# Kernel optimization log

Measured on AMD Instinct MI355X. Metric: run time of the kernel, lower is better.

## Reference

```python
import jax, jax.numpy as jnp
import numpy as np

B, D, H, NG = 8192, 2048, 2048, 7  # batch, input_size, hidden_size, num gate networks


def setup_inputs() -> dict:
    key = jax.random.key(0)
    ks = jax.random.split(key, 7)
    hx = jax.random.normal(ks[0], (B, D), dtype=jnp.float32)
    cx1 = jax.random.normal(ks[1], (B, H), dtype=jnp.float32)
    cx2 = jax.random.normal(ks[2], (B, H), dtype=jnp.float32)
    tj = jax.random.uniform(ks[3], (B, 1), dtype=jnp.float32)
    dt = jax.random.uniform(ks[4], (B, 1), dtype=jnp.float32)
    # fused weights for the 7 gate/decay networks, order: i1,i2,f1,f2,o,z,d
    W = jax.random.normal(ks[5], (D, NG * H), dtype=jnp.float32) * (1.0 / np.sqrt(D))
    b = jax.random.normal(ks[6], (NG * H,), dtype=jnp.float32) * 0.01
    return {"hx": hx, "cx1": cx1, "cx2": cx2, "tj": tj, "dt": dt, "W": W, "b": b}


def reference(hx, cx1, cx2, tj, dt, W, b):
    # One fused GEMM for all 7 gate networks, then split.
    g = hx @ W + b  # [B, 7H]
    i1, i2, f1, f2, o, z_raw, d_raw = [g[:, k * H:(k + 1) * H] for k in range(NG)]
    sig = jax.nn.sigmoid
    i1, i2, f1, f2, o = sig(i1), sig(i2), sig(f1), sig(f2), sig(o)
    z = jnp.tanh(z_raw)                 # Tanh(LC_z(hx)) as in forward
    decay = jax.nn.softplus(d_raw)      # Decay_network: positive decay coeff
    cy1 = f1 * cx1 + i1 * z             # fast cell state
    cy2 = f2 * cx2 + i2 * z             # asymptotic cell state
    t = tj + dt
    # continuous-time decay: c(t) = cy2 + (cy1 - cy2) * exp(-decay * (t - tj))
    c_t = cy2 + (cy1 - cy2) * jnp.exp(-decay * (t - tj))
    h_t = o * jnp.tanh(c_t)             # get_h(t)
    return jnp.stack([cy1, cy2, h_t])   # [3, B, H]
```

## Files before the change

### kernel.cpp

```cpp
#include <hip/hip_runtime.h>
#include <hip/hip_bf16.h>
#include <stdint.h>


#define B_SZ 8192
#define D_SZ 2048
#define H_SZ 2048
#define NG   7
#define NW   (NG * H_SZ)
#define BM   256
#define BN   32
#define BK   32
#define NKST (D_SZ / BK)
#define NBX  (B_SZ / BM)
#define NBY  (H_SZ / BN)

#define WB_BYTES   ((size_t)NBY * NKST * 14336)
#define HXB_OFF    WB_BYTES
#define HXB_BYTES  ((size_t)NBX * NKST * 16384)
#define WS_NEEDED  (WB_BYTES + HXB_BYTES)

typedef __attribute__((ext_vector_type(8))) short bf16x8;
typedef __attribute__((ext_vector_type(4))) float f32x4;

__device__ __forceinline__ uint32_t cvtpk(float lo, float hi) {
    uint32_t r;
    asm("v_cvt_pk_bf16_f32 %0, %1, %2" : "=v"(r) : "v"(lo), "v"(hi));
    return r;
}
__device__ __forceinline__ void glds16(const void* g, void* l) {
    __builtin_amdgcn_global_load_lds(
        (const __attribute__((address_space(1))) uint32_t*)g,
        (__attribute__((address_space(3))) uint32_t*)l, 16, 0, 0);
}
__device__ __forceinline__ float sigmoidf_(float x) {
    return 1.0f / (1.0f + __expf(-x));
}
__device__ __forceinline__ float tanhf_(float x) {
    float ax = fabsf(x);
    float e = __expf(2.0f * ax);
    float t = 1.0f - 2.0f / (e + 1.0f);
    return copysignf(t, x);
}
__device__ __forceinline__ float softplusf_(float x) {
    return (x > 30.0f) ? x : __logf(1.0f + __expf(x));
}

__global__ __launch_bounds__(896) void conv_w(const float* __restrict__ W,
                                              char* __restrict__ wb)
{
    const int by = blockIdx.x >> 6;
    const int ks = blockIdx.x & 63;
    const int u  = threadIdx.x;
    const int r  = u >> 2;
    const int pc = u & 3;
    const int koct = pc ^ ((r >> 1) & 3);
    const int g  = r >> 5;
    const int n  = r & 31;
    const int col = g * H_SZ + by * BN + n;
    const float* src = W + (size_t)(ks * BK + koct * 8) * NW + col;
    float w0 = src[0];
    float w1 = src[(size_t)NW];
    float w2 = src[(size_t)2 * NW];
    float w3 = src[(size_t)3 * NW];
    float w4 = src[(size_t)4 * NW];
    float w5 = src[(size_t)5 * NW];
    float w6 = src[(size_t)6 * NW];
    float w7 = src[(size_t)7 * NW];
    uint4 o;
    o.x = cvtpk(w0, w1); o.y = cvtpk(w2, w3);
    o.z = cvtpk(w4, w5); o.w = cvtpk(w6, w7);
    *(uint4*)(wb + (size_t)blockIdx.x * 14336 + u * 16) = o;
}

__global__ __launch_bounds__(1024) void conv_hx(const float* __restrict__ hx,
                                                char* __restrict__ hxb)
{
    const int bx = blockIdx.x >> 6;
    const int ks = blockIdx.x & 63;
    const int u  = threadIdx.x;
    const int r  = u >> 2;
    const int pc = u & 3;
    const int koct = pc ^ ((r >> 1) & 3);
    const float* src = hx + (size_t)(bx * BM + r) * D_SZ + ks * BK + koct * 8;
    f32x4 a = *(const f32x4*)(src);
    f32x4 b = *(const f32x4*)(src + 4);
    uint4 o;
    o.x = cvtpk(a[0], a[1]); o.y = cvtpk(a[2], a[3]);
    o.z = cvtpk(b[0], b[1]); o.w = cvtpk(b[2], b[3]);
    *(uint4*)(hxb + (size_t)blockIdx.x * 16384 + u * 16) = o;
}

#define NTH3 512
#define BUFB 30720
#define NBUF 4

#define SB0 __builtin_amdgcn_sched_barrier(0)
#define WAIT_LGKM0 do {                                          \
    asm volatile("s_waitcnt lgkmcnt(0)" ::: "memory");           \
    SB0; } while (0)
#define WAIT_VM(N) do {                                          \
    asm volatile("s_waitcnt vmcnt(" #N ")" ::: "memory");        \
    __builtin_amdgcn_s_barrier();                                \
    SB0; } while (0)

__global__ __launch_bounds__(NTH3, 2) void lstm_bf16(
    const char* __restrict__ wb, const char* __restrict__ hxb,
    const float* __restrict__ cx1, const float* __restrict__ cx2,
    const float* __restrict__ dt, const float* __restrict__ bias,
    float* __restrict__ out)
{
    __shared__ char smem[NBUF * BUFB];

    const int tid  = threadIdx.x;
    const int lane = tid & 63;
    const int wid  = tid >> 6;
    const int wm   = wid >> 1;
    const int wn   = wid & 1;
    const int l15  = lane & 15;
    const int lg   = lane >> 4;

    const int b0  = blockIdx.x;
    const int swz = (b0 & 7) * 256 + (b0 >> 3);
    const int by2 = swz >> 6;
    const int rem = swz & 63;
    const int bx  = rem >> 1;
    const int by  = by2 * 2 + (rem & 1);
    const int gm0 = bx * BM;
    const int n0  = by * BN;

    const size_t hx_tile0 = (size_t)(bx * NKST) << 14;
    const size_t w_tile0  = (size_t)(by * NKST) * 14336;

    const int xch = (lg ^ ((l15 >> 1) & 3)) * 8;
    const uint32_t aAb = (uint32_t)(uintptr_t)(smem) + 2u * ((wm * 64 + l15) * 32 + xch);
    const uint32_t aBb = (uint32_t)(uintptr_t)(smem) + 16384u + 2u * ((wn * 16 + l15) * 32 + xch);
    const uint32_t aA0 = aAb,            aA1 = aAb + BUFB;
    const uint32_t aA2 = aAb + 2 * BUFB, aA3 = aAb + 3 * BUFB;
    const uint32_t aB0 = aBb,            aB1 = aBb + BUFB;
    const uint32_t aB2 = aBb + 2 * BUFB, aB3 = aBb + 3 * BUFB;

    const int lane16 = lane << 4;
    const char* hxp0 = hxb + hx_tile0 + (wid << 11) + lane16;
    const char* wbp0 = wb + w_tile0 + wid * 1792 + lane16;
    char* dA0 = smem + (wid << 11);            char* dB0 = smem + 16384 + wid * 1792;
    char* dA1 = dA0 + BUFB;                    char* dB1 = dB0 + BUFB;
    char* dA2 = dA0 + 2 * BUFB;                char* dB2 = dB0 + 2 * BUFB;
    char* dA3 = dA0 + 3 * BUFB;                char* dB3 = dB0 + 3 * BUFB;

    f32x4 acc[NG][4];
    #pragma unroll
    for (int g = 0; g < NG; ++g)
        #pragma unroll
        for (int mf = 0; mf < 4; ++mf)
            acc[g][mf] = (f32x4){0.f, 0.f, 0.f, 0.f};

    bf16x8 fA[2][4];
    bf16x8 fB[2][7];

    #define ISSUE_FRAGS(S, AA, AB) do {                                           \
        asm volatile("s_mov_b32 m0, -1" ::);                                      \
        asm volatile("ds_read_b128 %0, %1"                : "=v"(fA[S][0]) : "v"(AA)); \
        asm volatile("ds_read_b128 %0, %1 offset:1024"    : "=v"(fA[S][1]) : "v"(AA)); \
        asm volatile("ds_read_b128 %0, %1 offset:2048"    : "=v"(fA[S][2]) : "v"(AA)); \
        asm volatile("ds_read_b128 %0, %1 offset:3072"    : "=v"(fA[S][3]) : "v"(AA)); \
        asm volatile("ds_read_b128 %0, %1"                : "=v"(fB[S][0]) : "v"(AB)); \
        asm volatile("ds_read_b128 %0, %1 offset:2048"    : "=v"(fB[S][1]) : "v"(AB)); \
        asm volatile("ds_read_b128 %0, %1 offset:4096"    : "=v"(fB[S][2]) : "v"(AB)); \
        asm volatile("ds_read_b128 %0, %1 offset:6144"    : "=v"(fB[S][3]) : "v"(AB)); \
        asm volatile("ds_read_b128 %0, %1 offset:8192"    : "=v"(fB[S][4]) : "v"(AB)); \
        asm volatile("ds_read_b128 %0, %1 offset:10240"   : "=v"(fB[S][5]) : "v"(AB)); \
        asm volatile("ds_read_b128 %0, %1 offset:12288"   : "=v"(fB[S][6]) : "v"(AB)); \
        SB0; } while (0)

    #define CLUSTER(S) do {                                                       \
        __builtin_amdgcn_s_setprio(1);                                            \
        _Pragma("unroll")                                                         \
        for (int g_ = 0; g_ < NG; ++g_)                                           \
            _Pragma("unroll")                                                     \
            for (int mf_ = 0; mf_ < 4; ++mf_)                                     \
                acc[g_][mf_] = __builtin_amdgcn_mfma_f32_16x16x32_bf16(           \
                    fA[S][mf_], fB[S][g_], acc[g_][mf_], 0, 0, 0);                \
        __builtin_amdgcn_s_setprio(0);                                            \
        SB0; } while (0)

    #define STAGE_C(c) do {                                                       \
        glds16(hxp, dA##c); glds16(hxp + 1024, dA##c + 1024);                     \
        glds16(wbp, dB##c);                                                       \
        if (lane < 48) glds16(wbp + 1024, dB##c + 1024);                          \
        hxp += 16384; wbp += 14336; } while (0)

    #define STAGE_K(c, k) do {                                                    \
        glds16(hxp0 + (k) * 16384, dA##c);                                        \
        glds16(hxp0 + (k) * 16384 + 1024, dA##c + 1024);                          \
        glds16(wbp0 + (k) * 14336, dB##c);                                        \
        if (lane < 48) glds16(wbp0 + (k) * 14336 + 1024, dB##c + 1024);           \
    } while (0)

    #define K_STEP(CN, SCUR, SNXT, VMN, STG) do {                                 \
        WAIT_LGKM0;                 \
        WAIT_VM(VMN);               \
        ISSUE_FRAGS(SNXT, aA##CN, aB##CN);                                        \
        STG;                                                                      \
        SB0;                                                                      \
        CLUSTER(SCUR); } while (0)

    STAGE_K(0, 0);
    STAGE_K(1, 1);
    STAGE_K(2, 2);
    const char* hxp = hxp0 + 3 * 16384;
    const char* wbp = wbp0 + 3 * 14336;
    asm volatile("s_waitcnt vmcnt(8)" ::: "memory");
    __builtin_amdgcn_s_barrier();
    SB0;
    ISSUE_FRAGS(0, aA0, aB0);

    #pragma unroll 1
    for (int it = 0; it < 15; ++it) {
        K_STEP(1, 0, 1, 4, STAGE_C(3));
        K_STEP(2, 1, 0, 4, STAGE_C(0));
        K_STEP(3, 0, 1, 4, STAGE_C(1));
        K_STEP(0, 1, 0, 4, STAGE_C(2));
    }
    K_STEP(1, 0, 1, 4, STAGE_C(3));
    K_STEP(2, 1, 0, 4, (void)0);
    K_STEP(3, 0, 1, 0, (void)0);
    WAIT_LGKM0;
    CLUSTER(1);

    const size_t BH = (size_t)B_SZ * H_SZ;
    const int j = n0 + wn * 16 + l15;
    float bj[NG];
    #pragma unroll
    for (int g = 0; g < NG; ++g) bj[g] = bias[g * H_SZ + j];

    #pragma unroll
    for (int mf = 0; mf < 4; ++mf) {
        #pragma unroll
        for (int r = 0; r < 4; ++r) {
            int row = gm0 + wm * 64 + mf * 16 + lg * 4 + r;
            float dtv = dt[row];
            float i1 = sigmoidf_(acc[0][mf][r] + bj[0]);
            float i2 = sigmoidf_(acc[1][mf][r] + bj[1]);
            float f1 = sigmoidf_(acc[2][mf][r] + bj[2]);
            float f2 = sigmoidf_(acc[3][mf][r] + bj[3]);
            float o  = sigmoidf_(acc[4][mf][r] + bj[4]);
            float z  = tanhf_(acc[5][mf][r] + bj[5]);
            float dec = softplusf_(acc[6][mf][r] + bj[6]);
            size_t idx = (size_t)row * H_SZ + j;
            float c1 = cx1[idx], c2 = cx2[idx];
            float cy1 = f1 * c1 + i1 * z;
            float cy2 = f2 * c2 + i2 * z;
            float ct  = cy2 + (cy1 - cy2) * __expf(-dec * dtv);
            float ht  = o * tanhf_(ct);
            out[idx]          = cy1;
            out[BH + idx]     = cy2;
            out[2 * BH + idx] = ht;
        }
    }
}

#define NTH  512
#define LDP  40
__global__ __launch_bounds__(NTH, 2) void lstm_f32(
    const float* __restrict__ hx, const float* __restrict__ cx1,
    const float* __restrict__ cx2, const float* __restrict__ dt,
    const float* __restrict__ W, const float* __restrict__ bias,
    float* __restrict__ out)
{
    __shared__ ushort sA[BM * LDP];
    __shared__ ushort sB[NG * BN * LDP];

    const int tid = threadIdx.x;
    const int nwg = gridDim.x;
    const int cpx = nwg >> 3;
    const int b0  = blockIdx.x;
    const int swz = (b0 & 7) * cpx + (b0 >> 3);
    const int bx  = swz & 31;
    const int by  = swz >> 5;
    const int gm0 = bx * BM;
    const int n0  = by * BN;

    const int lane = tid & 63;
    const int wid  = tid >> 6;
    const int wm   = wid >> 1;
    const int wn   = wid & 1;
    const int l15  = lane & 15;
    const int lg   = lane >> 4;

    const int ar0 = tid >> 2,          aq0 = tid & 3;
    const int ar1 = (tid + 512) >> 2,  aq1 = tid & 3;
    const bool hasB = (tid < 448);
    const int bg  = tid >> 6;
    const int bkq = (tid >> 3) & 7;
    const int bnq = tid & 7;

    f32x4 pa[4];
    f32x4 pb[4];

    auto issue_loads = [&](int K0) {
        {
            const float* p = hx + (size_t)(gm0 + ar0) * D_SZ + K0 + aq0 * 8;
            pa[0] = *(const f32x4*)(p);
            pa[1] = *(const f32x4*)(p + 4);
        }
        {
            const float* p = hx + (size_t)(gm0 + ar1) * D_SZ + K0 + aq1 * 8;
            pa[2] = *(const f32x4*)(p);
            pa[3] = *(const f32x4*)(p + 4);
        }
        if (hasB) {
            const float* p = W + (size_t)(K0 + bkq * 4) * NW + bg * H_SZ + n0 + bnq * 4;
            pb[0] = *(const f32x4*)(p);
            pb[1] = *(const f32x4*)(p + NW);
            pb[2] = *(const f32x4*)(p + 2 * NW);
            pb[3] = *(const f32x4*)(p + 3 * NW);
        }
    };

    auto store_lds = [&]() {
        {
            uint4 u;
            u.x = cvtpk(pa[0][0], pa[0][1]); u.y = cvtpk(pa[0][2], pa[0][3]);
            u.z = cvtpk(pa[1][0], pa[1][1]); u.w = cvtpk(pa[1][2], pa[1][3]);
            *(uint4*)(&sA[ar0 * LDP + aq0 * 8]) = u;
        }
        {
            uint4 u;
            u.x = cvtpk(pa[2][0], pa[2][1]); u.y = cvtpk(pa[2][2], pa[2][3]);
            u.z = cvtpk(pa[3][0], pa[3][1]); u.w = cvtpk(pa[3][2], pa[3][3]);
            *(uint4*)(&sA[ar1 * LDP + aq1 * 8]) = u;
        }
        if (hasB) {
            #pragma unroll
            for (int jj = 0; jj < 4; ++jj) {
                uint2 v;
                v.x = cvtpk(pb[0][jj], pb[1][jj]);
                v.y = cvtpk(pb[2][jj], pb[3][jj]);
                *(uint2*)(&sB[(bg * BN + bnq * 4 + jj) * LDP + bkq * 4]) = v;
            }
        }
    };

    f32x4 acc[NG][4];
    #pragma unroll
    for (int g = 0; g < NG; ++g)
        #pragma unroll
        for (int mf = 0; mf < 4; ++mf)
            acc[g][mf] = (f32x4){0.f, 0.f, 0.f, 0.f};

    int aoff[4];
    #pragma unroll
    for (int mf = 0; mf < 4; ++mf)
        aoff[mf] = (wm * 64 + mf * 16 + l15) * LDP + lg * 8;
    int boff[NG];
    #pragma unroll
    for (int g = 0; g < NG; ++g)
        boff[g] = (g * BN + wn * 16 + l15) * LDP + lg * 8;

    issue_loads(0);
    for (int kk = 0; kk < NKST; ++kk) {
        store_lds();
        __syncthreads();
        if (kk + 1 < NKST) issue_loads((kk + 1) * BK);

        bf16x8 af[4];
        #pragma unroll
        for (int mf = 0; mf < 4; ++mf)
            af[mf] = *(const bf16x8*)(&sA[aoff[mf]]);
        #pragma unroll
        for (int g = 0; g < NG; ++g) {
            bf16x8 bfr = *(const bf16x8*)(&sB[boff[g]]);
            #pragma unroll
            for (int mf = 0; mf < 4; ++mf)
                acc[g][mf] = __builtin_amdgcn_mfma_f32_16x16x32_bf16(
                    af[mf], bfr, acc[g][mf], 0, 0, 0);
        }
        __syncthreads();
    }

    const size_t BH = (size_t)B_SZ * H_SZ;
    const int j = n0 + wn * 16 + l15;
    float bj[NG];
    #pragma unroll
    for (int g = 0; g < NG; ++g) bj[g] = bias[g * H_SZ + j];

    #pragma unroll
    for (int mf = 0; mf < 4; ++mf) {
        #pragma unroll
        for (int r = 0; r < 4; ++r) {
            int row = gm0 + wm * 64 + mf * 16 + lg * 4 + r;
            float dtv = dt[row];
            float i1 = sigmoidf_(acc[0][mf][r] + bj[0]);
            float i2 = sigmoidf_(acc[1][mf][r] + bj[1]);
            float f1 = sigmoidf_(acc[2][mf][r] + bj[2]);
            float f2 = sigmoidf_(acc[3][mf][r] + bj[3]);
            float o  = sigmoidf_(acc[4][mf][r] + bj[4]);
            float z  = tanhf_(acc[5][mf][r] + bj[5]);
            float dec = softplusf_(acc[6][mf][r] + bj[6]);
            size_t idx = (size_t)row * H_SZ + j;
            float c1 = cx1[idx], c2 = cx2[idx];
            float cy1 = f1 * c1 + i1 * z;
            float cy2 = f2 * c2 + i2 * z;
            float ct  = cy2 + (cy1 - cy2) * __expf(-dec * dtv);
            float ht  = o * tanhf_(ct);
            out[idx]          = cy1;
            out[BH + idx]     = cy2;
            out[2 * BH + idx] = ht;
        }
    }
}

extern "C" void kernel_launch(void* const* d_in, const int* in_sizes, int n_in,
                              void* d_out, int out_size, void* d_ws, size_t ws_size,
                              hipStream_t stream) {
    const float* hx  = (const float*)d_in[0];
    const float* cx1 = (const float*)d_in[1];
    const float* cx2 = (const float*)d_in[2];
    const float* dt  = (const float*)d_in[4];
    const float* W   = (const float*)d_in[5];
    const float* b   = (const float*)d_in[6];
    float* out = (float*)d_out;

    if (ws_size >= WS_NEEDED) {
        char* wb  = (char*)d_ws;
        char* hxb = (char*)d_ws + HXB_OFF;
        conv_w<<<dim3(NBY * NKST), dim3(896), 0, stream>>>(W, wb);
        conv_hx<<<dim3(NBX * NKST), dim3(1024), 0, stream>>>(hx, hxb);
        lstm_bf16<<<dim3(NBX * NBY), dim3(NTH3), 0, stream>>>(
            wb, hxb, cx1, cx2, dt, b, out);
    } else {
        lstm_f32<<<dim3(NBX * NBY), dim3(NTH), 0, stream>>>(
            hx, cx1, cx2, dt, W, b, out);
    }
}
```

Baseline: 612.1 us.

## Split LDS fragment prefetch into per-row-fragment waits to cut register double-buffering

```diff
diff --git a/kernel.cpp b/kernel.cpp
--- a/kernel.cpp
+++ b/kernel.cpp
@@ -93,16 +93,8 @@
 
 #define NTH3 512
 #define BUFB 30720
-#define NBUF 4
 
 #define SB0 __builtin_amdgcn_sched_barrier(0)
-#define WAIT_LGKM0 do {                                          \
-    asm volatile("s_waitcnt lgkmcnt(0)" ::: "memory");           \
-    SB0; } while (0)
-#define WAIT_VM(N) do {                                          \
-    asm volatile("s_waitcnt vmcnt(" #N ")" ::: "memory");        \
-    __builtin_amdgcn_s_barrier();                                \
-    SB0; } while (0)
 
 __global__ __launch_bounds__(NTH3, 2) void lstm_bf16(
     const char* __restrict__ wb, const char* __restrict__ hxb,
@@ -110,7 +102,7 @@
     const float* __restrict__ dt, const float* __restrict__ bias,
     float* __restrict__ out)
 {
-    __shared__ char smem[NBUF * BUFB];
+    __shared__ char smem[4 * BUFB];
 
     const int tid  = threadIdx.x;
     const int lane = tid & 63;
@@ -129,20 +121,17 @@
     const int gm0 = bx * BM;
     const int n0  = by * BN;
 
-    const size_t hx_tile0 = (size_t)(bx * NKST) << 14;
-    const size_t w_tile0  = (size_t)(by * NKST) * 14336;
-
     const int xch = (lg ^ ((l15 >> 1) & 3)) * 8;
-    const uint32_t aAb = (uint32_t)(uintptr_t)(smem) + 2u * ((wm * 64 + l15) * 32 + xch);
-    const uint32_t aBb = (uint32_t)(uintptr_t)(smem) + 16384u + 2u * ((wn * 16 + l15) * 32 + xch);
+    const uint32_t aAb = (uint32_t)(uintptr_t)smem + 2u * ((wm * 64 + l15) * 32 + xch);
+    const uint32_t aBb = (uint32_t)(uintptr_t)smem + 16384u + 2u * ((wn * 16 + l15) * 32 + xch);
     const uint32_t aA0 = aAb,            aA1 = aAb + BUFB;
     const uint32_t aA2 = aAb + 2 * BUFB, aA3 = aAb + 3 * BUFB;
     const uint32_t aB0 = aBb,            aB1 = aBb + BUFB;
     const uint32_t aB2 = aBb + 2 * BUFB, aB3 = aBb + 3 * BUFB;
 
     const int lane16 = lane << 4;
-    const char* hxp0 = hxb + hx_tile0 + (wid << 11) + lane16;
-    const char* wbp0 = wb + w_tile0 + wid * 1792 + lane16;
+    const char* hxp0 = hxb + (((size_t)(bx * NKST)) << 14) + (wid << 11) + lane16;
+    const char* wbp0 = wb + (size_t)(by * NKST) * 14336 + wid * 1792 + lane16;
     char* dA0 = smem + (wid << 11);            char* dB0 = smem + 16384 + wid * 1792;
     char* dA1 = dA0 + BUFB;                    char* dB1 = dB0 + BUFB;
     char* dA2 = dA0 + 2 * BUFB;                char* dB2 = dB0 + 2 * BUFB;
@@ -155,55 +144,79 @@
         for (int mf = 0; mf < 4; ++mf)
             acc[g][mf] = (f32x4){0.f, 0.f, 0.f, 0.f};
 
-    bf16x8 fA[2][4];
-    bf16x8 fB[2][7];
-
-    #define ISSUE_FRAGS(S, AA, AB) do {                                           \
-        asm volatile("s_mov_b32 m0, -1" ::);                                      \
-        asm volatile("ds_read_b128 %0, %1"                : "=v"(fA[S][0]) : "v"(AA)); \
-        asm volatile("ds_read_b128 %0, %1 offset:1024"    : "=v"(fA[S][1]) : "v"(AA)); \
-        asm volatile("ds_read_b128 %0, %1 offset:2048"    : "=v"(fA[S][2]) : "v"(AA)); \
-        asm volatile("ds_read_b128 %0, %1 offset:3072"    : "=v"(fA[S][3]) : "v"(AA)); \
-        asm volatile("ds_read_b128 %0, %1"                : "=v"(fB[S][0]) : "v"(AB)); \
-        asm volatile("ds_read_b128 %0, %1 offset:2048"    : "=v"(fB[S][1]) : "v"(AB)); \
-        asm volatile("ds_read_b128 %0, %1 offset:4096"    : "=v"(fB[S][2]) : "v"(AB)); \
-        asm volatile("ds_read_b128 %0, %1 offset:6144"    : "=v"(fB[S][3]) : "v"(AB)); \
-        asm volatile("ds_read_b128 %0, %1 offset:8192"    : "=v"(fB[S][4]) : "v"(AB)); \
-        asm volatile("ds_read_b128 %0, %1 offset:10240"   : "=v"(fB[S][5]) : "v"(AB)); \
-        asm volatile("ds_read_b128 %0, %1 offset:12288"   : "=v"(fB[S][6]) : "v"(AB)); \
-        SB0; } while (0)
-
-    #define CLUSTER(S) do {                                                       \
-        __builtin_amdgcn_s_setprio(1);                                            \
-        _Pragma("unroll")                                                         \
-        for (int g_ = 0; g_ < NG; ++g_)                                           \
-            _Pragma("unroll")                                                     \
-            for (int mf_ = 0; mf_ < 4; ++mf_)                                     \
-                acc[g_][mf_] = __builtin_amdgcn_mfma_f32_16x16x32_bf16(           \
-                    fA[S][mf_], fB[S][g_], acc[g_][mf_], 0, 0, 0);                \
-        __builtin_amdgcn_s_setprio(0);                                            \
-        SB0; } while (0)
-
-    #define STAGE_C(c) do {                                                       \
-        glds16(hxp, dA##c); glds16(hxp + 1024, dA##c + 1024);                     \
-        glds16(wbp, dB##c);                                                       \
-        if (lane < 48) glds16(wbp + 1024, dB##c + 1024);                          \
-        hxp += 16384; wbp += 14336; } while (0)
-
-    #define STAGE_K(c, k) do {                                                    \
-        glds16(hxp0 + (k) * 16384, dA##c);                                        \
-        glds16(hxp0 + (k) * 16384 + 1024, dA##c + 1024);                          \
-        glds16(wbp0 + (k) * 14336, dB##c);                                        \
-        if (lane < 48) glds16(wbp0 + (k) * 14336 + 1024, dB##c + 1024);           \
-    } while (0)
-
-    #define K_STEP(CN, SCUR, SNXT, VMN, STG) do {                                 \
-        WAIT_LGKM0;                 \
-        WAIT_VM(VMN);               \
-        ISSUE_FRAGS(SNXT, aA##CN, aB##CN);                                        \
-        STG;                                                                      \
-        SB0;                                                                      \
-        CLUSTER(SCUR); } while (0)
+    bf16x8 fBE[NG], fBO[NG];
+    bf16x8 fA0E, fA0O, fA1, fA2, fA3;
+
+    #define ISSUE_A123(AAc) do {                                                   \
+        asm volatile("ds_read_b128 %0, %1 offset:1024" : "=&v"(fA1) : "v"(AAc));   \
+        asm volatile("ds_read_b128 %0, %1 offset:2048" : "=&v"(fA2) : "v"(AAc));   \
+        asm volatile("ds_read_b128 %0, %1 offset:3072" : "=&v"(fA3) : "v"(AAc));   \
+    } while (0)
+
+    #define ISSUE_NEXT(ABn, AAn, FBN, FA0N) do {                                   \
+        asm volatile("ds_read_b128 %0, %1"               : "=&v"(FBN[0]) : "v"(ABn)); \
+        asm volatile("ds_read_b128 %0, %1 offset:2048"   : "=&v"(FBN[1]) : "v"(ABn)); \
+        asm volatile("ds_read_b128 %0, %1 offset:4096"   : "=&v"(FBN[2]) : "v"(ABn)); \
+        asm volatile("ds_read_b128 %0, %1 offset:6144"   : "=&v"(FBN[3]) : "v"(ABn)); \
+        asm volatile("ds_read_b128 %0, %1 offset:8192"   : "=&v"(FBN[4]) : "v"(ABn)); \
+        asm volatile("ds_read_b128 %0, %1 offset:10240"  : "=&v"(FBN[5]) : "v"(ABn)); \
+        asm volatile("ds_read_b128 %0, %1 offset:12288"  : "=&v"(FBN[6]) : "v"(ABn)); \
+        asm volatile("ds_read_b128 %0, %1"               : "=&v"(FA0N)   : "v"(AAn)); \
+    } while (0)
+
+    #define CLUSTER(FA, FBC, MF, LGN) do {                                         \
+        asm volatile("s_waitcnt lgkmcnt(" #LGN ")" ::: "memory");                  \
+        SB0;                                                                       \
+        __builtin_amdgcn_s_setprio(1);                                             \
+        _Pragma("unroll")                                                          \
+        for (int g_ = 0; g_ < NG; ++g_)                                            \
+            acc[g_][MF] = __builtin_amdgcn_mfma_f32_16x16x32_bf16(                 \
+                FA, FBC[g_], acc[g_][MF], 0, 0, 0);                                \
+        __builtin_amdgcn_s_setprio(0);                                             \
+        SB0;                                                                       \
+    } while (0)
+
+    #define STAGE(SC) do {                                                         \
+        glds16(hxp, dA##SC); glds16(hxp + 1024, dA##SC + 1024);                    \
+        glds16(wbp, dB##SC);                                                       \
+        if (lane < 48) glds16(wbp + 1024, dB##SC + 1024);                          \
+        hxp += 16384; wbp += 14336;                                                \
+    } while (0)
+
+    #define STAGE_K(SC, K) do {                                                    \
+        glds16(hxp0 + (K) * 16384, dA##SC);                                        \
+        glds16(hxp0 + (K) * 16384 + 1024, dA##SC + 1024);                          \
+        glds16(wbp0 + (K) * 14336, dB##SC);                                        \
+        if (lane < 48) glds16(wbp0 + (K) * 14336 + 1024, dB##SC + 1024);           \
+    } while (0)
+
+    #define STEP_S(AAc, ABn, AAn, FBC, FBN, FA0C, FA0N, SC, VMN)  do {             \
+        asm volatile("s_waitcnt vmcnt(" #VMN ")" ::: "memory");                    \
+        __builtin_amdgcn_s_barrier();                                              \
+        SB0;                                                                       \
+        ISSUE_A123(AAc);                                                           \
+        ISSUE_NEXT(ABn, AAn, FBN, FA0N);                                           \
+        SB0;                                                                       \
+        STAGE(SC);                                                                 \
+        SB0;                                                                       \
+        CLUSTER(FA0C, FBC, 0, 11);                                                 \
+        CLUSTER(fA1,  FBC, 1, 10);                                                 \
+        CLUSTER(fA2,  FBC, 2, 9);                                                  \
+        CLUSTER(fA3,  FBC, 3, 8);                                                  \
+    } while (0)
+
+    #define STEP_N(AAc, ABn, AAn, FBC, FBN, FA0C, FA0N, VMN)  do {                 \
+        asm volatile("s_waitcnt vmcnt(" #VMN ")" ::: "memory");                    \
+        __builtin_amdgcn_s_barrier();                                              \
+        SB0;                                                                       \
+        ISSUE_A123(AAc);                                                           \
+        ISSUE_NEXT(ABn, AAn, FBN, FA0N);                                           \
+        SB0;                                                                       \
+        CLUSTER(FA0C, FBC, 0, 11);                                                 \
+        CLUSTER(fA1,  FBC, 1, 10);                                                 \
+        CLUSTER(fA2,  FBC, 2, 9);                                                  \
+        CLUSTER(fA3,  FBC, 3, 8);                                                  \
+    } while (0)
 
     STAGE_K(0, 0);
     STAGE_K(1, 1);
@@ -213,20 +226,25 @@
     asm volatile("s_waitcnt vmcnt(8)" ::: "memory");
     __builtin_amdgcn_s_barrier();
     SB0;
-    ISSUE_FRAGS(0, aA0, aB0);
+    ISSUE_NEXT(aB0, aA0, fBE, fA0E);
+    SB0;
 
     #pragma unroll 1
     for (int it = 0; it < 15; ++it) {
-        K_STEP(1, 0, 1, 4, STAGE_C(3));
-        K_STEP(2, 1, 0, 4, STAGE_C(0));
-        K_STEP(3, 0, 1, 4, STAGE_C(1));
-        K_STEP(0, 1, 0, 4, STAGE_C(2));
+        STEP_S(aA0, aB1, aA1, fBE, fBO, fA0E, fA0O, 3, 4);
+        STEP_S(aA1, aB2, aA2, fBO, fBE, fA0O, fA0E, 0, 4);
+        STEP_S(aA2, aB3, aA3, fBE, fBO, fA0E, fA0O, 1, 4);
+        STEP_S(aA3, aB0, aA0, fBO, fBE, fA0O, fA0E, 2, 4);
     }
-    K_STEP(1, 0, 1, 4, STAGE_C(3));
-    K_STEP(2, 1, 0, 4, (void)0);
-    K_STEP(3, 0, 1, 0, (void)0);
-    WAIT_LGKM0;
-    CLUSTER(1);
+    STEP_S(aA0, aB1, aA1, fBE, fBO, fA0E, fA0O, 3, 4);
+    STEP_N(aA1, aB2, aA2, fBO, fBE, fA0O, fA0E, 4);
+    STEP_N(aA2, aB3, aA3, fBE, fBO, fA0E, fA0O, 0);
+    ISSUE_A123(aA3);
+    SB0;
+    CLUSTER(fA0O, fBO, 0, 3);
+    CLUSTER(fA1,  fBO, 1, 2);
+    CLUSTER(fA2,  fBO, 2, 1);
+    CLUSTER(fA3,  fBO, 3, 0);
 
     const size_t BH = (size_t)B_SZ * H_SZ;
     const int j = n0 + wn * 16 + l15;
```

Result: faster. 533.8 us (median of 2 runs) (-12.8%).
